# Kernel tuning notes

Hardware: AMD Instinct MI355X
Metric: run time of the kernel (lower is better)

The kernel has to match this reference:

```python
import jax, jax.numpy as jnp
import numpy as np

N_NODES = 10000
N_EDGES = 100000
DIM = 768
NEG_SLOPE = 0.2  # PyG GATConv default


def gat_conv(x, src, dst, W, att_src, att_dst, bias, num_nodes):
    """Single-head PyG-style GATConv. src/dst already include self-loops."""
    h = x @ W                                  # [N, D]
    a_s = h @ att_src                          # [N]
    a_d = h @ att_dst                          # [N]
    e = jax.nn.leaky_relu(a_s[src] + a_d[dst], NEG_SLOPE)  # [E']
    # segment softmax over edges sharing the same destination node
    m = jax.ops.segment_max(e, dst, num_segments=num_nodes)  # [N]
    e = jnp.exp(e - m[dst])
    denom = jax.ops.segment_sum(e, dst, num_segments=num_nodes)  # [N]
    alpha = e / denom[dst]                     # [E']
    msg = alpha[:, None] * h[src]              # [E', D]
    out = jax.ops.segment_sum(msg, dst, num_segments=num_nodes)  # [N, D]
    return out + bias


def setup_inputs() -> dict:
    key = jax.random.key(0)
    ks = jax.random.split(key, 12)
    s = 1.0 / np.sqrt(DIM)
    inp = {
        "x": jax.random.normal(ks[0], (N_NODES, DIM), dtype=jnp.float32),
        "edge_index": jax.random.randint(ks[1], (2, N_EDGES), 0, N_NODES, dtype=jnp.int64),
        "W1": jax.random.normal(ks[2], (DIM, DIM), dtype=jnp.float32) * s,
        "att_src1": jax.random.normal(ks[3], (DIM,), dtype=jnp.float32) * s,
        "att_dst1": jax.random.normal(ks[4], (DIM,), dtype=jnp.float32) * s,
        "b1": jnp.zeros((DIM,), dtype=jnp.float32),
        "W2": jax.random.normal(ks[5], (DIM, DIM), dtype=jnp.float32) * s,
        "att_src2": jax.random.normal(ks[6], (DIM,), dtype=jnp.float32) * s,
        "att_dst2": jax.random.normal(ks[7], (DIM,), dtype=jnp.float32) * s,
        "b2": jnp.zeros((DIM,), dtype=jnp.float32),
    }
    return inp


def reference(x, edge_index, W1, att_src1, att_dst1, b1, W2, att_src2, att_dst2, b2):
    n = x.shape[0]
    # PyG GATConv default add_self_loops=True
    loops = jnp.arange(n, dtype=edge_index.dtype)
    src = jnp.concatenate([edge_index[0], loops])
    dst = jnp.concatenate([edge_index[1], loops])
    h = gat_conv(x, src, dst, W1, att_src1, att_dst1, b1, n)
    h = jax.nn.relu(h)
    # dropout p=0.0 in eval -> identity
    out = gat_conv(h, src, dst, W2, att_src2, att_dst2, b2, n)
    return out
```

## Files before the change

### kernel.cpp

```cpp
#include <hip/hip_runtime.h>

#define DIM 768
#define NEG_SLOPE 0.2f
#define MAXDEG 64

typedef unsigned short ushort_t;
typedef short short8 __attribute__((ext_vector_type(8)));
typedef float floatx4 __attribute__((ext_vector_type(4)));

__device__ __forceinline__ ushort_t f32_to_bf16(float f) {
  unsigned int b = __float_as_uint(f);
  b += 0x7FFFu + ((b >> 16) & 1u);
  return (ushort_t)(b >> 16);
}
__device__ __forceinline__ float bf16_to_f32(ushort_t u) {
  return __uint_as_float(((unsigned int)u) << 16);
}
__device__ __forceinline__ float bf16lo(unsigned int u) {
  return __uint_as_float(u << 16);
}
__device__ __forceinline__ float bf16hi(unsigned int u) {
  return __uint_as_float(u & 0xFFFF0000u);
}
__device__ __forceinline__ unsigned int pack_bf16x2(float lo, float hi) {
  return ((unsigned int)f32_to_bf16(lo)) | (((unsigned int)f32_to_bf16(hi)) << 16);
}

__device__ __forceinline__ void gl2lds16(const ushort_t* g, ushort_t* l) {
  __builtin_amdgcn_global_load_lds(
      (const __attribute__((address_space(1))) void*)g,
      (__attribute__((address_space(3))) void*)l, 16, 0, 0);
}

__global__ __launch_bounds__(256)
void prep_kernel(const float* __restrict__ x, ushort_t* __restrict__ xb, int n4,
                 const float* __restrict__ W1, ushort_t* __restrict__ wT1,
                 const float* __restrict__ W2, ushort_t* __restrict__ wT2,
                 int* __restrict__ zbase, int nz4) {
  __shared__ ushort_t tile[64][65];
  int b = blockIdx.x;
  int t = threadIdx.x;
  if (b < 288) {
    int mat = b / 144;
    int ti = b - mat * 144;
    int tr = (ti / 12) * 64;
    int tc = (ti % 12) * 64;
    const float* W = mat ? W2 : W1;
    ushort_t* wT = mat ? wT2 : wT1;
    int lr = t >> 4, lc4 = (t & 15) * 4;
#pragma unroll
    for (int p = 0; p < 4; ++p) {
      int row = lr + p * 16;
      float4 v = *(const float4*)(W + (size_t)(tr + row) * DIM + tc + lc4);
      tile[row][lc4 + 0] = f32_to_bf16(v.x);
      tile[row][lc4 + 1] = f32_to_bf16(v.y);
      tile[row][lc4 + 2] = f32_to_bf16(v.z);
      tile[row][lc4 + 3] = f32_to_bf16(v.w);
    }
    __syncthreads();
    int n = t & 63, kb = (t >> 6) * 16;
    ushort_t tmp[16];
#pragma unroll
    for (int i = 0; i < 16; ++i) tmp[i] = tile[kb + i][n];
    ushort_t* dst = wT + (size_t)(tc + n) * DIM + tr + kb;
    *(uint4*)(dst) = *(const uint4*)(&tmp[0]);
    *(uint4*)(dst + 8) = *(const uint4*)(&tmp[8]);
  } else {
    int i = (b - 288) * 256 + t;
    if (i < n4) {
      float4 v = ((const float4*)x)[i];
      ushort4 o;
      o.x = f32_to_bf16(v.x); o.y = f32_to_bf16(v.y);
      o.z = f32_to_bf16(v.z); o.w = f32_to_bf16(v.w);
      ((ushort4*)xb)[i] = o;
    }
    if (i < nz4) {
      ((uint4*)zbase)[i] = make_uint4(0, 0, 0, 0);
    }
  }
}

__global__ void csr_kernel(const int* __restrict__ ei, int* __restrict__ deg,
                           int* __restrict__ col, int E, int Etot) {
  int e = blockIdx.x * 256 + threadIdx.x;
  if (e >= Etot) return;
  int s, d;
  if (e < E) { s = ei[e]; d = ei[E + e]; }
  else       { s = e - E; d = e - E; }
  int slot = atomicAdd(&deg[d], 1);
  if (slot < MAXDEG) col[(size_t)d * MAXDEG + slot] = s;
}

__global__ __launch_bounds__(256)
void gemm_kernel(const ushort_t* __restrict__ A, const ushort_t* __restrict__ Bt,
                 const float* __restrict__ att_s, const float* __restrict__ att_d,
                 float* __restrict__ a_s, float* __restrict__ a_d,
                 ushort_t* __restrict__ Hb, int M, int MBLK) {
  const int K = DIM;
  __shared__ __align__(16) ushort_t As[2][128 * 64];
  __shared__ __align__(16) ushort_t Bs[2][128 * 64];
  int b = blockIdx.x;
  int x = b & 7, sidx = b >> 3;
  int m_local = sidx / 6, nblk = sidx - m_local * 6;
  int mblk = x * MBLK + m_local;
  if (mblk * 128 >= M) return;
  int m0 = mblk * 128, n0 = nblk * 128;
  int tid = threadIdx.x;
  int wave = tid >> 6, lane = tid & 63;
  int quad = lane >> 4, l16 = lane & 15;
  int wr = wave >> 1, wc = wave & 1;

  floatx4 acc[4][4];
  const floatx4 fzero = {0.f, 0.f, 0.f, 0.f};
#pragma unroll
  for (int i = 0; i < 4; ++i)
#pragma unroll
    for (int j = 0; j < 4; ++j) acc[i][j] = fzero;

  int lr = lane >> 3, lc = lane & 7;
  const ushort_t* gA[4];
  const ushort_t* gB[4];
  ushort_t* lA[4];
  ushort_t* lB[4];
#pragma unroll
  for (int t = 0; t < 4; ++t) {
    int r = t * 32 + wave * 8 + lr;
    int g = lc ^ (r & 7);
    gA[t] = A + (size_t)min(m0 + r, M - 1) * K + g * 8;
    gB[t] = Bt + (size_t)(n0 + r) * K + g * 8;
    lA[t] = &As[0][(t * 32 + wave * 8) * 64];
    lB[t] = &Bs[0][(t * 32 + wave * 8) * 64];
  }

#define GEMM_STAGE(k0_, buf_)                                         \
  {                                                                   \
    _Pragma("unroll")                                                 \
    for (int t = 0; t < 4; ++t) gl2lds16(gA[t] + (k0_), lA[t] + (buf_)*8192); \
    _Pragma("unroll")                                                 \
    for (int t = 0; t < 4; ++t) gl2lds16(gB[t] + (k0_), lB[t] + (buf_)*8192); \
  }

  GEMM_STAGE(0, 0);
  __syncthreads();
  int cur = 0;

  for (int k0 = 0; k0 < K; k0 += 64) {
    if (k0 + 64 < K) GEMM_STAGE(k0 + 64, cur ^ 1);
    const ushort_t* Ab = &As[cur][0];
    const ushort_t* Bb = &Bs[cur][0];
#pragma unroll
    for (int h = 0; h < 2; ++h) {
      short8 af[4], bfr[4];
#pragma unroll
      for (int i = 0; i < 4; ++i) {
        int ra = wr * 64 + i * 16 + l16;
        af[i] = *(const short8*)(Ab + ra * 64 + ((((h << 2) | quad)) ^ (ra & 7)) * 8);
      }
#pragma unroll
      for (int j = 0; j < 4; ++j) {
        int rb = wc * 64 + j * 16 + l16;
        bfr[j] = *(const short8*)(Bb + rb * 64 + ((((h << 2) | quad)) ^ (rb & 7)) * 8);
      }
#pragma unroll
      for (int i = 0; i < 4; ++i)
#pragma unroll
        for (int j = 0; j < 4; ++j)
          acc[i][j] = __builtin_amdgcn_mfma_f32_16x16x32_bf16(af[i], bfr[j], acc[i][j], 0, 0, 0);
    }
    __syncthreads();
    cur ^= 1;
  }

  float avs[4], avd[4];
#pragma unroll
  for (int j = 0; j < 4; ++j) {
    int c = n0 + wc * 64 + j * 16 + l16;
    avs[j] = att_s[c];
    avd[j] = att_d[c];
  }

#pragma unroll
  for (int i = 0; i < 4; ++i) {
#pragma unroll
    for (int r2 = 0; r2 < 4; ++r2) {
      int row = m0 + wr * 64 + i * 16 + quad * 4 + r2;
      bool valid = row < M;
      float pvs = 0.f, pvd = 0.f;
#pragma unroll
      for (int j = 0; j < 4; ++j) {
        float v = acc[i][j][r2];
        if (valid) Hb[(size_t)row * DIM + n0 + wc * 64 + j * 16 + l16] = f32_to_bf16(v);
        pvs = fmaf(v, avs[j], pvs);
        pvd = fmaf(v, avd[j], pvd);
      }
#pragma unroll
      for (int off = 1; off < 16; off <<= 1) {
        pvs += __shfl_xor(pvs, off, 64);
        pvd += __shfl_xor(pvd, off, 64);
      }
      if (valid && l16 == 0) {
        atomicAdd(a_s + row, pvs);
        atomicAdd(a_d + row, pvd);
      }
    }
  }
}

__global__ __launch_bounds__(256)
void aggregate_kernel(const ushort_t* __restrict__ h, const float* __restrict__ a_s,
                      const float* __restrict__ a_d, const int* __restrict__ deg,
                      const int* __restrict__ col, const float* __restrict__ bias,
                      float* __restrict__ out_f32, ushort_t* __restrict__ out_bf16,
                      int relu_mode, int N) {
  int wave = threadIdx.x >> 6, lane = threadIdx.x & 63;
  int node = blockIdx.x * 4 + wave;
  if (node >= N) return;
  int dg = min(deg[node], MAXDEG);
  int base = node * MAXDEG;
  float ad = a_d[node];

  bool has = lane < dg;
  int sc = col[base + min(lane, dg - 1)];
  float v = a_s[sc] + ad;
  v = (v > 0.f) ? v : NEG_SLOPE * v;
  float vmax = v;
#pragma unroll
  for (int off = 32; off > 0; off >>= 1) vmax = fmaxf(vmax, __shfl_xor(vmax, off, 64));
  float ex = has ? __expf(v - vmax) : 0.f;
  float ssum = ex;
#pragma unroll
  for (int off = 32; off > 0; off >>= 1) ssum += __shfl_xor(ssum, off, 64);
  float al = ex * (1.f / ssum);

  float acc8[8];
  float acc4[4];
#pragma unroll
  for (int k = 0; k < 8; ++k) acc8[k] = 0.f;
#pragma unroll
  for (int k = 0; k < 4; ++k) acc4[k] = 0.f;

  uint4 uA[4], uB[4];
  ushort4 tA[4], tB[4];
  float wA[4], wB[4];

#define GAT_LOADC(b_, u_, t_, w_)                                     \
  {                                                                   \
    _Pragma("unroll")                                                 \
    for (int q = 0; q < 4; ++q) {                                     \
      int j_ = (b_) + q;                                              \
      w_[q] = __shfl(al, j_, 64);                                     \
      int s_ = __shfl(sc, j_, 64);                                    \
      const ushort_t* hr_ = h + (size_t)s_ * DIM;                     \
      u_[q] = *(const uint4*)(hr_ + lane * 8);                        \
      t_[q] = *(const ushort4*)(hr_ + 512 + lane * 4);                \
    }                                                                 \
  }

#define GAT_FMAC(u_, t_, w_)                                          \
  {                                                                   \
    _Pragma("unroll")                                                 \
    for (int q = 0; q < 4; ++q) {                                     \
      float w = w_[q];                                                \
      acc8[0] = fmaf(w, bf16lo(u_[q].x), acc8[0]);                    \
      acc8[1] = fmaf(w, bf16hi(u_[q].x), acc8[1]);                    \
      acc8[2] = fmaf(w, bf16lo(u_[q].y), acc8[2]);                    \
      acc8[3] = fmaf(w, bf16hi(u_[q].y), acc8[3]);                    \
      acc8[4] = fmaf(w, bf16lo(u_[q].z), acc8[4]);                    \
      acc8[5] = fmaf(w, bf16hi(u_[q].z), acc8[5]);                    \
      acc8[6] = fmaf(w, bf16lo(u_[q].w), acc8[6]);                    \
      acc8[7] = fmaf(w, bf16hi(u_[q].w), acc8[7]);                    \
      acc4[0] = fmaf(w, bf16_to_f32(t_[q].x), acc4[0]);               \
      acc4[1] = fmaf(w, bf16_to_f32(t_[q].y), acc4[1]);               \
      acc4[2] = fmaf(w, bf16_to_f32(t_[q].z), acc4[2]);               \
      acc4[3] = fmaf(w, bf16_to_f32(t_[q].w), acc4[3]);               \
    }                                                                 \
  }

  int dgc = (dg + 3) & ~3;
  GAT_LOADC(0, uA, tA, wA);
  for (int b = 0; b < dgc; b += 8) {
    if (b + 4 < dgc) GAT_LOADC(b + 4, uB, tB, wB);
    GAT_FMAC(uA, tA, wA);
    if (b + 8 < dgc) GAT_LOADC(b + 8, uA, tA, wA);
    if (b + 4 < dgc) GAT_FMAC(uB, tB, wB);
  }

  size_t ob = (size_t)node * DIM;
  int c8 = lane * 8, c4 = 512 + lane * 4;
  float4 b0 = *(const float4*)(bias + c8);
  float4 b1 = *(const float4*)(bias + c8 + 4);
  float4 b2 = *(const float4*)(bias + c4);
  float o[12];
  o[0] = acc8[0] + b0.x; o[1] = acc8[1] + b0.y;
  o[2] = acc8[2] + b0.z; o[3] = acc8[3] + b0.w;
  o[4] = acc8[4] + b1.x; o[5] = acc8[5] + b1.y;
  o[6] = acc8[6] + b1.z; o[7] = acc8[7] + b1.w;
  o[8] = acc4[0] + b2.x; o[9] = acc4[1] + b2.y;
  o[10] = acc4[2] + b2.z; o[11] = acc4[3] + b2.w;
  if (relu_mode) {
#pragma unroll
    for (int k = 0; k < 12; ++k) o[k] = fmaxf(o[k], 0.f);
    uint4 s0;
    s0.x = pack_bf16x2(o[0], o[1]);
    s0.y = pack_bf16x2(o[2], o[3]);
    s0.z = pack_bf16x2(o[4], o[5]);
    s0.w = pack_bf16x2(o[6], o[7]);
    *(uint4*)(out_bf16 + ob + c8) = s0;
    uint2 s1;
    s1.x = pack_bf16x2(o[8], o[9]);
    s1.y = pack_bf16x2(o[10], o[11]);
    *(uint2*)(out_bf16 + ob + c4) = s1;
  } else {
    *(float4*)(out_f32 + ob + c8) = make_float4(o[0], o[1], o[2], o[3]);
    *(float4*)(out_f32 + ob + c8 + 4) = make_float4(o[4], o[5], o[6], o[7]);
    *(float4*)(out_f32 + ob + c4) = make_float4(o[8], o[9], o[10], o[11]);
  }
}

extern "C" void kernel_launch(void* const* d_in, const int* in_sizes, int n_in,
                              void* d_out, int out_size, void* d_ws, size_t ws_size,
                              hipStream_t stream) {
  const float* x   = (const float*)d_in[0];
  const int*   ei  = (const int*)d_in[1];
  const float* W1  = (const float*)d_in[2];
  const float* as1 = (const float*)d_in[3];
  const float* ad1 = (const float*)d_in[4];
  const float* b1  = (const float*)d_in[5];
  const float* W2  = (const float*)d_in[6];
  const float* as2 = (const float*)d_in[7];
  const float* ad2 = (const float*)d_in[8];
  const float* b2  = (const float*)d_in[9];

  const int N = in_sizes[0] / DIM;
  const int E = in_sizes[1] / 2;
  const int Etot = E + N;

  char* p = (char*)d_ws;
  auto alloc = [&](size_t bytes) {
    char* q = p;
    p += (bytes + 255) & ~(size_t)255;
    return q;
  };
  ushort_t* Hb     = (ushort_t*)alloc((size_t)N * DIM * 2);
  ushort_t* xb     = (ushort_t*)alloc((size_t)N * DIM * 2);
  ushort_t* wT1    = (ushort_t*)alloc((size_t)DIM * DIM * 2);
  ushort_t* wT2    = (ushort_t*)alloc((size_t)DIM * DIM * 2);
  int*      zbase  = (int*)alloc((size_t)5 * N * 4 + 16);
  int*      deg    = zbase;
  float*    a_s1   = (float*)(zbase + N);
  float*    a_d1   = (float*)(zbase + 2 * N);
  float*    a_s2   = (float*)(zbase + 3 * N);
  float*    a_d2   = (float*)(zbase + 4 * N);
  int*      col    = (int*)alloc((size_t)N * MAXDEG * 4);

  int n4 = N * DIM / 4;
  int nz4 = (5 * N + 3) / 4;
  int prep_blocks = 288 + (n4 + 255) / 256;
  prep_kernel<<<prep_blocks, 256, 0, stream>>>(x, xb, n4, W1, wT1, W2, wT2,
                                               zbase, nz4);
  csr_kernel<<<(Etot + 255) / 256, 256, 0, stream>>>(ei, deg, col, E, Etot);

  int MB = (N + 127) / 128;
  int MBLK = (MB + 7) / 8;
  int gemm_blocks = 8 * MBLK * 6;
  int agg_blocks = (N + 3) / 4;

  gemm_kernel<<<gemm_blocks, 256, 0, stream>>>(xb, wT1, as1, ad1, a_s1, a_d1, Hb, N, MBLK);
  aggregate_kernel<<<agg_blocks, 256, 0, stream>>>(Hb, a_s1, a_d1, deg, col, b1,
                                                   nullptr, xb, 1, N);
  gemm_kernel<<<gemm_blocks, 256, 0, stream>>>(xb, wT2, as2, ad2, a_s2, a_d2, Hb, N, MBLK);
  aggregate_kernel<<<agg_blocks, 256, 0, stream>>>(Hb, a_s2, a_d2, deg, col, b2,
                                                   (float*)d_out, nullptr, 0, N);
}
```

Measured before the change: 200.5 us.

## Fold CSR build into GEMM launch and split aggregation into alpha and gather

CSR construction now runs as extra blocks of the first GEMM launch, which removes one launch and lets the edge scatter overlap the matmul. Aggregation is split into two kernels: one computes the softmax weights per node and stores them, plus padded column indices, in a new alpha buffer. A persistent-style gather kernel with half the blocks then loops over nodes and prefetches the next node's degree, columns and weights while accumulating the current one. This adds one launch per layer and extra global traffic for the alpha array, in exchange for overlapping the softmax and index loads with the gather.

```diff
diff --git a/kernel.cpp b/kernel.cpp
--- a/kernel.cpp
+++ b/kernel.cpp
@@ -80,26 +80,28 @@
   }
 }
 
-__global__ void csr_kernel(const int* __restrict__ ei, int* __restrict__ deg,
-                           int* __restrict__ col, int E, int Etot) {
-  int e = blockIdx.x * 256 + threadIdx.x;
-  if (e >= Etot) return;
-  int s, d;
-  if (e < E) { s = ei[e]; d = ei[E + e]; }
-  else       { s = e - E; d = e - E; }
-  int slot = atomicAdd(&deg[d], 1);
-  if (slot < MAXDEG) col[(size_t)d * MAXDEG + slot] = s;
-}
-
 __global__ __launch_bounds__(256)
 void gemm_kernel(const ushort_t* __restrict__ A, const ushort_t* __restrict__ Bt,
                  const float* __restrict__ att_s, const float* __restrict__ att_d,
                  float* __restrict__ a_s, float* __restrict__ a_d,
-                 ushort_t* __restrict__ Hb, int M, int MBLK) {
+                 ushort_t* __restrict__ Hb, int M, int MBLK,
+                 const int* __restrict__ ei, int* __restrict__ degw,
+                 int* __restrict__ colw, int E, int Etot, int gemmBlocks) {
   const int K = DIM;
   __shared__ __align__(16) ushort_t As[2][128 * 64];
   __shared__ __align__(16) ushort_t Bs[2][128 * 64];
   int b = blockIdx.x;
+  if (b >= gemmBlocks) {
+    int e = (b - gemmBlocks) * 256 + threadIdx.x;
+    if (e < Etot) {
+      int s, d;
+      if (e < E) { s = ei[e]; d = ei[E + e]; }
+      else       { s = e - E; d = e - E; }
+      int slot = atomicAdd(&degw[d], 1);
+      if (slot < MAXDEG) colw[(size_t)d * MAXDEG + slot] = s;
+    }
+    return;
+  }
   int x = b & 7, sidx = b >> 3;
   int m_local = sidx / 6, nblk = sidx - m_local * 6;
   int mblk = x * MBLK + m_local;
@@ -207,11 +209,9 @@
 }
 
 __global__ __launch_bounds__(256)
-void aggregate_kernel(const ushort_t* __restrict__ h, const float* __restrict__ a_s,
-                      const float* __restrict__ a_d, const int* __restrict__ deg,
-                      const int* __restrict__ col, const float* __restrict__ bias,
-                      float* __restrict__ out_f32, ushort_t* __restrict__ out_bf16,
-                      int relu_mode, int N) {
+void alpha_kernel(const float* __restrict__ a_s, const float* __restrict__ a_d,
+                  const int* __restrict__ deg, int* __restrict__ col,
+                  float* __restrict__ alpha, int N) {
   int wave = threadIdx.x >> 6, lane = threadIdx.x & 63;
   int node = blockIdx.x * 4 + wave;
   if (node >= N) return;
@@ -230,14 +230,24 @@
   float ssum = ex;
 #pragma unroll
   for (int off = 32; off > 0; off >>= 1) ssum += __shfl_xor(ssum, off, 64);
-  float al = ex * (1.f / ssum);
-
-  float acc8[8];
-  float acc4[4];
-#pragma unroll
-  for (int k = 0; k < 8; ++k) acc8[k] = 0.f;
-#pragma unroll
-  for (int k = 0; k < 4; ++k) acc4[k] = 0.f;
+  alpha[base + lane] = ex * (1.f / ssum);
+  if (!has) col[base + lane] = sc;
+}
+
+__global__ __launch_bounds__(256)
+void gather_kernel(const ushort_t* __restrict__ h, const float* __restrict__ alpha,
+                   const int* __restrict__ deg, const int* __restrict__ col,
+                   const float* __restrict__ bias,
+                   float* __restrict__ out_f32, ushort_t* __restrict__ out_bf16,
+                   int relu_mode, int N) {
+  int lane = threadIdx.x & 63;
+  int wstride = gridDim.x * 4;
+  int node = blockIdx.x * 4 + (threadIdx.x >> 6);
+  if (node >= N) return;
+
+  int dg = min(deg[node], MAXDEG);
+  int sc = col[node * MAXDEG + lane];
+  float al = alpha[node * MAXDEG + lane];
 
   uint4 uA[4], uB[4];
   ushort4 tA[4], tB[4];
@@ -276,44 +286,66 @@
     }                                                                 \
   }
 
-  int dgc = (dg + 3) & ~3;
-  GAT_LOADC(0, uA, tA, wA);
-  for (int b = 0; b < dgc; b += 8) {
-    if (b + 4 < dgc) GAT_LOADC(b + 4, uB, tB, wB);
-    GAT_FMAC(uA, tA, wA);
-    if (b + 8 < dgc) GAT_LOADC(b + 8, uA, tA, wA);
-    if (b + 4 < dgc) GAT_FMAC(uB, tB, wB);
-  }
-
-  size_t ob = (size_t)node * DIM;
   int c8 = lane * 8, c4 = 512 + lane * 4;
   float4 b0 = *(const float4*)(bias + c8);
   float4 b1 = *(const float4*)(bias + c8 + 4);
   float4 b2 = *(const float4*)(bias + c4);
-  float o[12];
-  o[0] = acc8[0] + b0.x; o[1] = acc8[1] + b0.y;
-  o[2] = acc8[2] + b0.z; o[3] = acc8[3] + b0.w;
-  o[4] = acc8[4] + b1.x; o[5] = acc8[5] + b1.y;
-  o[6] = acc8[6] + b1.z; o[7] = acc8[7] + b1.w;
-  o[8] = acc4[0] + b2.x; o[9] = acc4[1] + b2.y;
-  o[10] = acc4[2] + b2.z; o[11] = acc4[3] + b2.w;
-  if (relu_mode) {
-#pragma unroll
-    for (int k = 0; k < 12; ++k) o[k] = fmaxf(o[k], 0.f);
-    uint4 s0;
-    s0.x = pack_bf16x2(o[0], o[1]);
-    s0.y = pack_bf16x2(o[2], o[3]);
-    s0.z = pack_bf16x2(o[4], o[5]);
-    s0.w = pack_bf16x2(o[6], o[7]);
-    *(uint4*)(out_bf16 + ob + c8) = s0;
-    uint2 s1;
-    s1.x = pack_bf16x2(o[8], o[9]);
-    s1.y = pack_bf16x2(o[10], o[11]);
-    *(uint2*)(out_bf16 + ob + c4) = s1;
-  } else {
-    *(float4*)(out_f32 + ob + c8) = make_float4(o[0], o[1], o[2], o[3]);
-    *(float4*)(out_f32 + ob + c8 + 4) = make_float4(o[4], o[5], o[6], o[7]);
-    *(float4*)(out_f32 + ob + c4) = make_float4(o[8], o[9], o[10], o[11]);
+
+  while (node < N) {
+    int nn = node + wstride;
+    float acc8[8];
+    float acc4[4];
+#pragma unroll
+    for (int k = 0; k < 8; ++k) acc8[k] = 0.f;
+#pragma unroll
+    for (int k = 0; k < 4; ++k) acc4[k] = 0.f;
+
+    int dgc = (dg + 3) & ~3;
+    GAT_LOADC(0, uA, tA, wA);
+
+    int dg2 = 0, sc2 = 0;
+    float al2 = 0.f;
+    if (nn < N) {
+      dg2 = min(deg[nn], MAXDEG);
+      sc2 = col[nn * MAXDEG + lane];
+      al2 = alpha[nn * MAXDEG + lane];
+    }
+
+    for (int b = 0; b < dgc; b += 8) {
+      if (b + 4 < dgc) GAT_LOADC(b + 4, uB, tB, wB);
+      GAT_FMAC(uA, tA, wA);
+      if (b + 8 < dgc) GAT_LOADC(b + 8, uA, tA, wA);
+      if (b + 4 < dgc) GAT_FMAC(uB, tB, wB);
+    }
+
+    size_t ob = (size_t)node * DIM;
+    float o[12];
+    o[0] = acc8[0] + b0.x; o[1] = acc8[1] + b0.y;
+    o[2] = acc8[2] + b0.z; o[3] = acc8[3] + b0.w;
+    o[4] = acc8[4] + b1.x; o[5] = acc8[5] + b1.y;
+    o[6] = acc8[6] + b1.z; o[7] = acc8[7] + b1.w;
+    o[8] = acc4[0] + b2.x; o[9] = acc4[1] + b2.y;
+    o[10] = acc4[2] + b2.z; o[11] = acc4[3] + b2.w;
+    if (relu_mode) {
+#pragma unroll
+      for (int k = 0; k < 12; ++k) o[k] = fmaxf(o[k], 0.f);
+      uint4 s0;
+      s0.x = pack_bf16x2(o[0], o[1]);
+      s0.y = pack_bf16x2(o[2], o[3]);
+      s0.z = pack_bf16x2(o[4], o[5]);
+      s0.w = pack_bf16x2(o[6], o[7]);
+      *(uint4*)(out_bf16 + ob + c8) = s0;
+      uint2 s1;
+      s1.x = pack_bf16x2(o[8], o[9]);
+      s1.y = pack_bf16x2(o[10], o[11]);
+      *(uint2*)(out_bf16 + ob + c4) = s1;
+    } else {
+      *(float4*)(out_f32 + ob + c8) = make_float4(o[0], o[1], o[2], o[3]);
+      *(float4*)(out_f32 + ob + c8 + 4) = make_float4(o[4], o[5], o[6], o[7]);
+      *(float4*)(out_f32 + ob + c4) = make_float4(o[8], o[9], o[10], o[11]);
+    }
+
+    node = nn; dg = dg2; sc = sc2; al = al2;
   }
 }
 
@@ -352,23 +384,29 @@
   float*    a_s2   = (float*)(zbase + 3 * N);
   float*    a_d2   = (float*)(zbase + 4 * N);
   int*      col    = (int*)alloc((size_t)N * MAXDEG * 4);
+  float*    alpha  = (float*)alloc((size_t)N * MAXDEG * 4);
 
   int n4 = N * DIM / 4;
   int nz4 = (5 * N + 3) / 4;
   int prep_blocks = 288 + (n4 + 255) / 256;
   prep_kernel<<<prep_blocks, 256, 0, stream>>>(x, xb, n4, W1, wT1, W2, wT2,
                                                zbase, nz4);
-  csr_kernel<<<(Etot + 255) / 256, 256, 0, stream>>>(ei, deg, col, E, Etot);
 
   int MB = (N + 127) / 128;
   int MBLK = (MB + 7) / 8;
   int gemm_blocks = 8 * MBLK * 6;
-  int agg_blocks = (N + 3) / 4;
-
-  gemm_kernel<<<gemm_blocks, 256, 0, stream>>>(xb, wT1, as1, ad1, a_s1, a_d1, Hb, N, MBLK);
-  aggregate_kernel<<<agg_blocks, 256, 0, stream>>>(Hb, a_s1, a_d1, deg, col, b1,
+  int csr_blocks = (Etot + 255) / 256;
+  int alpha_blocks = (N + 3) / 4;
+  int gather_blocks = (N + 7) / 8;
+
+  gemm_kernel<<<gemm_blocks + csr_blocks, 256, 0, stream>>>(
+      xb, wT1, as1, ad1, a_s1, a_d1, Hb, N, MBLK, ei, deg, col, E, Etot, gemm_blocks);
+  alpha_kernel<<<alpha_blocks, 256, 0, stream>>>(a_s1, a_d1, deg, col, alpha, N);
+  gather_kernel<<<gather_blocks, 256, 0, stream>>>(Hb, alpha, deg, col, b1,
                                                    nullptr, xb, 1, N);
-  gemm_kernel<<<gemm_blocks, 256, 0, stream>>>(xb, wT2, as2, ad2, a_s2, a_d2, Hb, N, MBLK);
-  aggregate_kernel<<<agg_blocks, 256, 0, stream>>>(Hb, a_s2, a_d2, deg, col, b2,
+  gemm_kernel<<<gemm_blocks, 256, 0, stream>>>(
+      xb, wT2, as2, ad2, a_s2, a_d2, Hb, N, MBLK, ei, deg, col, E, 0, gemm_blocks);
+  alpha_kernel<<<alpha_blocks, 256, 0, stream>>>(a_s2, a_d2, deg, col, alpha, N);
+  gather_kernel<<<gather_blocks, 256, 0, stream>>>(Hb, alpha, deg, col, b2,
                                                    (float*)d_out, nullptr, 0, N);
 }
```

Result: slower. 207.2 us (+3.3%).

## Fuse all GAT stages into one persistent kernel with grid barriers

Applied to the files above, without the earlier changes.

Replaces the six separate kernel launches (prep, CSR build, two GEMMs, two aggregations) with a single persistent mega-kernel that steps through the phases using a software grid-wide barrier. Zeroing of the degree and attention buffers moves to a hipMemsetAsync. The aim is to remove launch gaps and inter-kernel drain/fill costs. In exchange, the GEMM and aggregation phases become grid-stride loops over a fixed grid, which changes occupancy and load balance. The spin barrier is also only safe if all blocks are co-resident, and the grid size (G = 8*MBLK*6, 480 blocks here) is not checked against residency limits.

```diff
diff --git a/kernel.cpp b/kernel.cpp
--- a/kernel.cpp
+++ b/kernel.cpp
@@ -32,105 +32,78 @@
       (__attribute__((address_space(3))) void*)l, 16, 0, 0);
 }
 
-__global__ __launch_bounds__(256)
-void prep_kernel(const float* __restrict__ x, ushort_t* __restrict__ xb, int n4,
-                 const float* __restrict__ W1, ushort_t* __restrict__ wT1,
-                 const float* __restrict__ W2, ushort_t* __restrict__ wT2,
-                 int* __restrict__ zbase, int nz4) {
-  __shared__ ushort_t tile[64][65];
-  int b = blockIdx.x;
-  int t = threadIdx.x;
-  if (b < 288) {
-    int mat = b / 144;
-    int ti = b - mat * 144;
-    int tr = (ti / 12) * 64;
-    int tc = (ti % 12) * 64;
-    const float* W = mat ? W2 : W1;
-    ushort_t* wT = mat ? wT2 : wT1;
-    int lr = t >> 4, lc4 = (t & 15) * 4;
-#pragma unroll
-    for (int p = 0; p < 4; ++p) {
-      int row = lr + p * 16;
-      float4 v = *(const float4*)(W + (size_t)(tr + row) * DIM + tc + lc4);
-      tile[row][lc4 + 0] = f32_to_bf16(v.x);
-      tile[row][lc4 + 1] = f32_to_bf16(v.y);
-      tile[row][lc4 + 2] = f32_to_bf16(v.z);
-      tile[row][lc4 + 3] = f32_to_bf16(v.w);
-    }
-    __syncthreads();
-    int n = t & 63, kb = (t >> 6) * 16;
-    ushort_t tmp[16];
-#pragma unroll
-    for (int i = 0; i < 16; ++i) tmp[i] = tile[kb + i][n];
-    ushort_t* dst = wT + (size_t)(tc + n) * DIM + tr + kb;
-    *(uint4*)(dst) = *(const uint4*)(&tmp[0]);
-    *(uint4*)(dst + 8) = *(const uint4*)(&tmp[8]);
-  } else {
-    int i = (b - 288) * 256 + t;
-    if (i < n4) {
-      float4 v = ((const float4*)x)[i];
-      ushort4 o;
-      o.x = f32_to_bf16(v.x); o.y = f32_to_bf16(v.y);
-      o.z = f32_to_bf16(v.z); o.w = f32_to_bf16(v.w);
-      ((ushort4*)xb)[i] = o;
-    }
-    if (i < nz4) {
-      ((uint4*)zbase)[i] = make_uint4(0, 0, 0, 0);
-    }
-  }
-}
-
-__global__ void csr_kernel(const int* __restrict__ ei, int* __restrict__ deg,
-                           int* __restrict__ col, int E, int Etot) {
-  int e = blockIdx.x * 256 + threadIdx.x;
-  if (e >= Etot) return;
-  int s, d;
-  if (e < E) { s = ei[e]; d = ei[E + e]; }
-  else       { s = e - E; d = e - E; }
-  int slot = atomicAdd(&deg[d], 1);
-  if (slot < MAXDEG) col[(size_t)d * MAXDEG + slot] = s;
-}
-
-__global__ __launch_bounds__(256)
-void gemm_kernel(const ushort_t* __restrict__ A, const ushort_t* __restrict__ Bt,
-                 const float* __restrict__ att_s, const float* __restrict__ att_d,
-                 float* __restrict__ a_s, float* __restrict__ a_d,
-                 ushort_t* __restrict__ Hb, int M, int MBLK) {
+__device__ __forceinline__ void grid_barrier(int* cnt, int* gen, int nblk) {
+  __syncthreads();
+  if (threadIdx.x == 0) {
+    __threadfence();
+    int g = __hip_atomic_load(gen, __ATOMIC_ACQUIRE, __HIP_MEMORY_SCOPE_AGENT);
+    int arrived = __hip_atomic_fetch_add(cnt, 1, __ATOMIC_ACQ_REL,
+                                         __HIP_MEMORY_SCOPE_AGENT);
+    if (arrived == nblk - 1) {
+      __hip_atomic_store(cnt, 0, __ATOMIC_RELAXED, __HIP_MEMORY_SCOPE_AGENT);
+      __hip_atomic_store(gen, g + 1, __ATOMIC_RELEASE, __HIP_MEMORY_SCOPE_AGENT);
+    } else {
+      while (__hip_atomic_load(gen, __ATOMIC_ACQUIRE,
+                               __HIP_MEMORY_SCOPE_AGENT) == g) {
+        __builtin_amdgcn_s_sleep(8);
+      }
+    }
+    __threadfence();
+  }
+  __syncthreads();
+}
+
+struct MegaArgs {
+  const float* x; const int* ei;
+  const float* W1; const float* as1; const float* ad1; const float* b1;
+  const float* W2; const float* as2; const float* ad2; const float* b2;
+  ushort_t* xb; ushort_t* wT1; ushort_t* wT2; ushort_t* Hb;
+  int* zbase; int* col;
+  float* out;
+  int N, E, Etot, MBLK, n4;
+};
+
+__device__ __forceinline__ void gemm_phase(
+    const ushort_t* __restrict__ A, const ushort_t* __restrict__ Bt,
+    const float* __restrict__ att_s, const float* __restrict__ att_d,
+    float* __restrict__ a_s, float* __restrict__ a_d,
+    ushort_t* __restrict__ Hb, int M, int MBLK,
+    ushort_t* AsBase, ushort_t* BsBase) {
   const int K = DIM;
-  __shared__ __align__(16) ushort_t As[2][128 * 64];
-  __shared__ __align__(16) ushort_t Bs[2][128 * 64];
-  int b = blockIdx.x;
-  int x = b & 7, sidx = b >> 3;
-  int m_local = sidx / 6, nblk = sidx - m_local * 6;
-  int mblk = x * MBLK + m_local;
-  if (mblk * 128 >= M) return;
-  int m0 = mblk * 128, n0 = nblk * 128;
+  int ntiles = 8 * MBLK * 6;
   int tid = threadIdx.x;
   int wave = tid >> 6, lane = tid & 63;
   int quad = lane >> 4, l16 = lane & 15;
   int wr = wave >> 1, wc = wave & 1;
-
-  floatx4 acc[4][4];
-  const floatx4 fzero = {0.f, 0.f, 0.f, 0.f};
-#pragma unroll
-  for (int i = 0; i < 4; ++i)
-#pragma unroll
-    for (int j = 0; j < 4; ++j) acc[i][j] = fzero;
-
   int lr = lane >> 3, lc = lane & 7;
-  const ushort_t* gA[4];
-  const ushort_t* gB[4];
-  ushort_t* lA[4];
-  ushort_t* lB[4];
-#pragma unroll
-  for (int t = 0; t < 4; ++t) {
-    int r = t * 32 + wave * 8 + lr;
-    int g = lc ^ (r & 7);
-    gA[t] = A + (size_t)min(m0 + r, M - 1) * K + g * 8;
-    gB[t] = Bt + (size_t)(n0 + r) * K + g * 8;
-    lA[t] = &As[0][(t * 32 + wave * 8) * 64];
-    lB[t] = &Bs[0][(t * 32 + wave * 8) * 64];
-  }
+
+  for (int b = blockIdx.x; b < ntiles; b += gridDim.x) {
+    int x = b & 7, sidx = b >> 3;
+    int m_local = sidx / 6, nblk = sidx - m_local * 6;
+    int mblk = x * MBLK + m_local;
+    if (mblk * 128 >= M) continue;
+    int m0 = mblk * 128, n0 = nblk * 128;
+
+    floatx4 acc[4][4];
+    const floatx4 fzero = {0.f, 0.f, 0.f, 0.f};
+#pragma unroll
+    for (int i = 0; i < 4; ++i)
+#pragma unroll
+      for (int j = 0; j < 4; ++j) acc[i][j] = fzero;
+
+    const ushort_t* gA[4];
+    const ushort_t* gB[4];
+    ushort_t* lA[4];
+    ushort_t* lB[4];
+#pragma unroll
+    for (int t = 0; t < 4; ++t) {
+      int r = t * 32 + wave * 8 + lr;
+      int g = lc ^ (r & 7);
+      gA[t] = A + (size_t)min(m0 + r, M - 1) * K + g * 8;
+      gB[t] = Bt + (size_t)(n0 + r) * K + g * 8;
+      lA[t] = AsBase + (t * 32 + wave * 8) * 64;
+      lB[t] = BsBase + (t * 32 + wave * 8) * 64;
+    }
 
 #define GEMM_STAGE(k0_, buf_)                                         \
   {                                                                   \
@@ -140,108 +113,117 @@
     for (int t = 0; t < 4; ++t) gl2lds16(gB[t] + (k0_), lB[t] + (buf_)*8192); \
   }
 
-  GEMM_STAGE(0, 0);
-  __syncthreads();
-  int cur = 0;
-
-  for (int k0 = 0; k0 < K; k0 += 64) {
-    if (k0 + 64 < K) GEMM_STAGE(k0 + 64, cur ^ 1);
-    const ushort_t* Ab = &As[cur][0];
-    const ushort_t* Bb = &Bs[cur][0];
-#pragma unroll
-    for (int h = 0; h < 2; ++h) {
-      short8 af[4], bfr[4];
-#pragma unroll
-      for (int i = 0; i < 4; ++i) {
-        int ra = wr * 64 + i * 16 + l16;
-        af[i] = *(const short8*)(Ab + ra * 64 + ((((h << 2) | quad)) ^ (ra & 7)) * 8);
+    GEMM_STAGE(0, 0);
+    __syncthreads();
+    int cur = 0;
+
+    for (int k0 = 0; k0 < K; k0 += 64) {
+      if (k0 + 64 < K) GEMM_STAGE(k0 + 64, cur ^ 1);
+      const ushort_t* Ab = AsBase + cur * 8192;
+      const ushort_t* Bb = BsBase + cur * 8192;
+#pragma unroll
+      for (int h = 0; h < 2; ++h) {
+        short8 af[4], bfr[4];
+#pragma unroll
+        for (int i = 0; i < 4; ++i) {
+          int ra = wr * 64 + i * 16 + l16;
+          af[i] = *(const short8*)(Ab + ra * 64 + ((((h << 2) | quad)) ^ (ra & 7)) * 8);
+        }
+#pragma unroll
+        for (int j = 0; j < 4; ++j) {
+          int rb = wc * 64 + j * 16 + l16;
+          bfr[j] = *(const short8*)(Bb + rb * 64 + ((((h << 2) | quad)) ^ (rb & 7)) * 8);
+        }
+#pragma unroll
+        for (int i = 0; i < 4; ++i)
+#pragma unroll
+          for (int j = 0; j < 4; ++j)
+            acc[i][j] = __builtin_amdgcn_mfma_f32_16x16x32_bf16(af[i], bfr[j], acc[i][j], 0, 0, 0);
       }
-#pragma unroll
-      for (int j = 0; j < 4; ++j) {
-        int rb = wc * 64 + j * 16 + l16;
-        bfr[j] = *(const short8*)(Bb + rb * 64 + ((((h << 2) | quad)) ^ (rb & 7)) * 8);
+      __syncthreads();
+      cur ^= 1;
+    }
+#undef GEMM_STAGE
+
+    float avs[4], avd[4];
+#pragma unroll
+    for (int j = 0; j < 4; ++j) {
+      int c = n0 + wc * 64 + j * 16 + l16;
+      avs[j] = att_s[c];
+      avd[j] = att_d[c];
+    }
+
+#pragma unroll
+    for (int i = 0; i < 4; ++i) {
+#pragma unroll
+      for (int r2 = 0; r2 < 4; ++r2) {
+        int row = m0 + wr * 64 + i * 16 + quad * 4 + r2;
+        bool valid = row < M;
+        float pvs = 0.f, pvd = 0.f;
+#pragma unroll
+        for (int j = 0; j < 4; ++j) {
+          float v = acc[i][j][r2];
+          if (valid) Hb[(size_t)row * DIM + n0 + wc * 64 + j * 16 + l16] = f32_to_bf16(v);
+          pvs = fmaf(v, avs[j], pvs);
+          pvd = fmaf(v, avd[j], pvd);
+        }
+#pragma unroll
+        for (int off = 1; off < 16; off <<= 1) {
+          pvs += __shfl_xor(pvs, off, 64);
+          pvd += __shfl_xor(pvd, off, 64);
+        }
+        if (valid && l16 == 0) {
+          atomicAdd(a_s + row, pvs);
+          atomicAdd(a_d + row, pvd);
+        }
       }
-#pragma unroll
-      for (int i = 0; i < 4; ++i)
-#pragma unroll
-        for (int j = 0; j < 4; ++j)
-          acc[i][j] = __builtin_amdgcn_mfma_f32_16x16x32_bf16(af[i], bfr[j], acc[i][j], 0, 0, 0);
-    }
-    __syncthreads();
-    cur ^= 1;
-  }
-
-  float avs[4], avd[4];
-#pragma unroll
-  for (int j = 0; j < 4; ++j) {
-    int c = n0 + wc * 64 + j * 16 + l16;
-    avs[j] = att_s[c];
-    avd[j] = att_d[c];
-  }
-
-#pragma unroll
-  for (int i = 0; i < 4; ++i) {
-#pragma unroll
-    for (int r2 = 0; r2 < 4; ++r2) {
-      int row = m0 + wr * 64 + i * 16 + quad * 4 + r2;
-      bool valid = row < M;
-      float pvs = 0.f, pvd = 0.f;
-#pragma unroll
-      for (int j = 0; j < 4; ++j) {
-        float v = acc[i][j][r2];
-        if (valid) Hb[(size_t)row * DIM + n0 + wc * 64 + j * 16 + l16] = f32_to_bf16(v);
-        pvs = fmaf(v, avs[j], pvs);
-        pvd = fmaf(v, avd[j], pvd);
-      }
-#pragma unroll
-      for (int off = 1; off < 16; off <<= 1) {
-        pvs += __shfl_xor(pvs, off, 64);
-        pvd += __shfl_xor(pvd, off, 64);
-      }
-      if (valid && l16 == 0) {
-        atomicAdd(a_s + row, pvs);
-        atomicAdd(a_d + row, pvd);
-      }
-    }
-  }
-}
-
-__global__ __launch_bounds__(256)
-void aggregate_kernel(const ushort_t* __restrict__ h, const float* __restrict__ a_s,
-                      const float* __restrict__ a_d, const int* __restrict__ deg,
-                      const int* __restrict__ col, const float* __restrict__ bias,
-                      float* __restrict__ out_f32, ushort_t* __restrict__ out_bf16,
-                      int relu_mode, int N) {
-  int wave = threadIdx.x >> 6, lane = threadIdx.x & 63;
-  int node = blockIdx.x * 4 + wave;
-  if (node >= N) return;
-  int dg = min(deg[node], MAXDEG);
-  int base = node * MAXDEG;
-  float ad = a_d[node];
-
-  bool has = lane < dg;
-  int sc = col[base + min(lane, dg - 1)];
-  float v = a_s[sc] + ad;
-  v = (v > 0.f) ? v : NEG_SLOPE * v;
-  float vmax = v;
-#pragma unroll
-  for (int off = 32; off > 0; off >>= 1) vmax = fmaxf(vmax, __shfl_xor(vmax, off, 64));
-  float ex = has ? __expf(v - vmax) : 0.f;
-  float ssum = ex;
-#pragma unroll
-  for (int off = 32; off > 0; off >>= 1) ssum += __shfl_xor(ssum, off, 64);
-  float al = ex * (1.f / ssum);
-
-  float acc8[8];
-  float acc4[4];
-#pragma unroll
-  for (int k = 0; k < 8; ++k) acc8[k] = 0.f;
-#pragma unroll
-  for (int k = 0; k < 4; ++k) acc4[k] = 0.f;
-
-  uint4 uA[4], uB[4];
-  ushort4 tA[4], tB[4];
-  float wA[4], wB[4];
+    }
+  }
+}
+
+__device__ __forceinline__ void agg_phase(
+    const ushort_t* __restrict__ h, const float* __restrict__ a_s,
+    float* a_d, int* deg,
+    const int* __restrict__ col, const float* __restrict__ bias,
+    float* __restrict__ out_f32, ushort_t* __restrict__ out_bf16,
+    int relu_mode, int N) {
+  int lane = threadIdx.x & 63;
+  int wave = threadIdx.x >> 6;
+  int c8 = lane * 8, c4 = 512 + lane * 4;
+  float4 b0 = *(const float4*)(bias + c8);
+  float4 b1v = *(const float4*)(bias + c8 + 4);
+  float4 b2v = *(const float4*)(bias + c4);
+
+  for (int node = blockIdx.x * 4 + wave; node < N; node += gridDim.x * 4) {
+    int dg = min(__hip_atomic_load(&deg[node], __ATOMIC_RELAXED,
+                                   __HIP_MEMORY_SCOPE_AGENT), MAXDEG);
+    int base = node * MAXDEG;
+    float ad = __hip_atomic_load(&a_d[node], __ATOMIC_RELAXED,
+                                 __HIP_MEMORY_SCOPE_AGENT);
+
+    bool has = lane < dg;
+    int sc = col[base + min(lane, dg - 1)];
+    float v = a_s[sc] + ad;
+    v = (v > 0.f) ? v : NEG_SLOPE * v;
+    float vmax = v;
+#pragma unroll
+    for (int off = 32; off > 0; off >>= 1) vmax = fmaxf(vmax, __shfl_xor(vmax, off, 64));
+    float ex = has ? __expf(v - vmax) : 0.f;
+    float ssum = ex;
+#pragma unroll
+    for (int off = 32; off > 0; off >>= 1) ssum += __shfl_xor(ssum, off, 64);
+    float al = ex * (1.f / ssum);
+
+    float acc8[8];
+    float acc4[4];
+#pragma unroll
+    for (int k = 0; k < 8; ++k) acc8[k] = 0.f;
+#pragma unroll
+    for (int k = 0; k < 4; ++k) acc4[k] = 0.f;
+
+    uint4 uA[4], uB[4];
+    ushort4 tA[4], tB[4];
+    float wA[4], wB[4];
 
 #define GAT_LOADC(b_, u_, t_, w_)                                     \
   {                                                                   \
@@ -276,45 +258,121 @@
     }                                                                 \
   }
 
-  int dgc = (dg + 3) & ~3;
-  GAT_LOADC(0, uA, tA, wA);
-  for (int b = 0; b < dgc; b += 8) {
-    if (b + 4 < dgc) GAT_LOADC(b + 4, uB, tB, wB);
-    GAT_FMAC(uA, tA, wA);
-    if (b + 8 < dgc) GAT_LOADC(b + 8, uA, tA, wA);
-    if (b + 4 < dgc) GAT_FMAC(uB, tB, wB);
-  }
-
-  size_t ob = (size_t)node * DIM;
-  int c8 = lane * 8, c4 = 512 + lane * 4;
-  float4 b0 = *(const float4*)(bias + c8);
-  float4 b1 = *(const float4*)(bias + c8 + 4);
-  float4 b2 = *(const float4*)(bias + c4);
-  float o[12];
-  o[0] = acc8[0] + b0.x; o[1] = acc8[1] + b0.y;
-  o[2] = acc8[2] + b0.z; o[3] = acc8[3] + b0.w;
-  o[4] = acc8[4] + b1.x; o[5] = acc8[5] + b1.y;
-  o[6] = acc8[6] + b1.z; o[7] = acc8[7] + b1.w;
-  o[8] = acc4[0] + b2.x; o[9] = acc4[1] + b2.y;
-  o[10] = acc4[2] + b2.z; o[11] = acc4[3] + b2.w;
-  if (relu_mode) {
-#pragma unroll
-    for (int k = 0; k < 12; ++k) o[k] = fmaxf(o[k], 0.f);
-    uint4 s0;
-    s0.x = pack_bf16x2(o[0], o[1]);
-    s0.y = pack_bf16x2(o[2], o[3]);
-    s0.z = pack_bf16x2(o[4], o[5]);
-    s0.w = pack_bf16x2(o[6], o[7]);
-    *(uint4*)(out_bf16 + ob + c8) = s0;
-    uint2 s1;
-    s1.x = pack_bf16x2(o[8], o[9]);
-    s1.y = pack_bf16x2(o[10], o[11]);
-    *(uint2*)(out_bf16 + ob + c4) = s1;
-  } else {
-    *(float4*)(out_f32 + ob + c8) = make_float4(o[0], o[1], o[2], o[3]);
-    *(float4*)(out_f32 + ob + c8 + 4) = make_float4(o[4], o[5], o[6], o[7]);
-    *(float4*)(out_f32 + ob + c4) = make_float4(o[8], o[9], o[10], o[11]);
-  }
+    int dgc = (dg + 3) & ~3;
+    GAT_LOADC(0, uA, tA, wA);
+    for (int bb = 0; bb < dgc; bb += 8) {
+      if (bb + 4 < dgc) GAT_LOADC(bb + 4, uB, tB, wB);
+      GAT_FMAC(uA, tA, wA);
+      if (bb + 8 < dgc) GAT_LOADC(bb + 8, uA, tA, wA);
+      if (bb + 4 < dgc) GAT_FMAC(uB, tB, wB);
+    }
+#undef GAT_LOADC
+#undef GAT_FMAC
+
+    size_t ob = (size_t)node * DIM;
+    float o[12];
+    o[0] = acc8[0] + b0.x; o[1] = acc8[1] + b0.y;
+    o[2] = acc8[2] + b0.z; o[3] = acc8[3] + b0.w;
+    o[4] = acc8[4] + b1v.x; o[5] = acc8[5] + b1v.y;
+    o[6] = acc8[6] + b1v.z; o[7] = acc8[7] + b1v.w;
+    o[8] = acc4[0] + b2v.x; o[9] = acc4[1] + b2v.y;
+    o[10] = acc4[2] + b2v.z; o[11] = acc4[3] + b2v.w;
+    if (relu_mode) {
+#pragma unroll
+      for (int k = 0; k < 12; ++k) o[k] = fmaxf(o[k], 0.f);
+      uint4 s0;
+      s0.x = pack_bf16x2(o[0], o[1]);
+      s0.y = pack_bf16x2(o[2], o[3]);
+      s0.z = pack_bf16x2(o[4], o[5]);
+      s0.w = pack_bf16x2(o[6], o[7]);
+      *(uint4*)(out_bf16 + ob + c8) = s0;
+      uint2 s1;
+      s1.x = pack_bf16x2(o[8], o[9]);
+      s1.y = pack_bf16x2(o[10], o[11]);
+      *(uint2*)(out_bf16 + ob + c4) = s1;
+    } else {
+      *(float4*)(out_f32 + ob + c8) = make_float4(o[0], o[1], o[2], o[3]);
+      *(float4*)(out_f32 + ob + c8 + 4) = make_float4(o[4], o[5], o[6], o[7]);
+      *(float4*)(out_f32 + ob + c4) = make_float4(o[8], o[9], o[10], o[11]);
+    }
+  }
+}
+
+__global__ __launch_bounds__(256, 2)
+void mega_kernel(MegaArgs a) {
+  __shared__ __align__(16) ushort_t As[2][128 * 64];
+  __shared__ __align__(16) ushort_t Bs[2][128 * 64];
+
+  int* deg    = a.zbase;
+  float* a_s1 = (float*)(a.zbase + a.N);
+  float* a_d1 = (float*)(a.zbase + 2 * a.N);
+  float* a_s2 = (float*)(a.zbase + 3 * a.N);
+  float* a_d2 = (float*)(a.zbase + 4 * a.N);
+  int* bcnt   = a.zbase + 5 * a.N;
+  int* bgen   = a.zbase + 5 * a.N + 1;
+  int nblk    = gridDim.x;
+
+  {
+    ushort_t (*tile)[65] = reinterpret_cast<ushort_t(*)[65]>(&As[0][0]);
+    int t = threadIdx.x;
+    for (int b = blockIdx.x; b < 288; b += gridDim.x) {
+      int mat = b / 144;
+      int ti = b - mat * 144;
+      int tr = (ti / 12) * 64;
+      int tc = (ti % 12) * 64;
+      const float* W = mat ? a.W2 : a.W1;
+      ushort_t* wT = mat ? a.wT2 : a.wT1;
+      int lr = t >> 4, lc4 = (t & 15) * 4;
+#pragma unroll
+      for (int p = 0; p < 4; ++p) {
+        int row = lr + p * 16;
+        float4 v = *(const float4*)(W + (size_t)(tr + row) * DIM + tc + lc4);
+        tile[row][lc4 + 0] = f32_to_bf16(v.x);
+        tile[row][lc4 + 1] = f32_to_bf16(v.y);
+        tile[row][lc4 + 2] = f32_to_bf16(v.z);
+        tile[row][lc4 + 3] = f32_to_bf16(v.w);
+      }
+      __syncthreads();
+      int n = t & 63, kb = (t >> 6) * 16;
+      ushort_t tmp[16];
+#pragma unroll
+      for (int i = 0; i < 16; ++i) tmp[i] = tile[kb + i][n];
+      ushort_t* dst = wT + (size_t)(tc + n) * DIM + tr + kb;
+      *(uint4*)(dst) = *(const uint4*)(&tmp[0]);
+      *(uint4*)(dst + 8) = *(const uint4*)(&tmp[8]);
+      __syncthreads();
+    }
+    for (int i = blockIdx.x * 256 + threadIdx.x; i < a.n4; i += gridDim.x * 256) {
+      float4 v = ((const float4*)a.x)[i];
+      ushort4 o;
+      o.x = f32_to_bf16(v.x); o.y = f32_to_bf16(v.y);
+      o.z = f32_to_bf16(v.z); o.w = f32_to_bf16(v.w);
+      ((ushort4*)a.xb)[i] = o;
+    }
+  }
+  grid_barrier(bcnt, bgen, nblk);
+
+  for (int e = blockIdx.x * 256 + threadIdx.x; e < a.Etot; e += gridDim.x * 256) {
+    int s, d;
+    if (e < a.E) { s = a.ei[e]; d = a.ei[a.E + e]; }
+    else         { s = e - a.E; d = e - a.E; }
+    int slot = atomicAdd(&deg[d], 1);
+    if (slot < MAXDEG) a.col[(size_t)d * MAXDEG + slot] = s;
+  }
+  grid_barrier(bcnt, bgen, nblk);
+
+  gemm_phase(a.xb, a.wT1, a.as1, a.ad1, a_s1, a_d1, a.Hb, a.N, a.MBLK,
+             &As[0][0], &Bs[0][0]);
+  grid_barrier(bcnt, bgen, nblk);
+
+  agg_phase(a.Hb, a_s1, a_d1, deg, a.col, a.b1, nullptr, a.xb, 1, a.N);
+  grid_barrier(bcnt, bgen, nblk);
+
+  gemm_phase(a.xb, a.wT2, a.as2, a.ad2, a_s2, a_d2, a.Hb, a.N, a.MBLK,
+             &As[0][0], &Bs[0][0]);
+  grid_barrier(bcnt, bgen, nblk);
+
+  agg_phase(a.Hb, a_s2, a_d2, deg, a.col, a.b2, a.out, nullptr, 0, a.N);
 }
 
 extern "C" void kernel_launch(void* const* d_in, const int* in_sizes, int n_in,
@@ -346,29 +404,22 @@
   ushort_t* wT1    = (ushort_t*)alloc((size_t)DIM * DIM * 2);
   ushort_t* wT2    = (ushort_t*)alloc((size_t)DIM * DIM * 2);
   int*      zbase  = (int*)alloc((size_t)5 * N * 4 + 16);
-  int*      deg    = zbase;
-  float*    a_s1   = (float*)(zbase + N);
-  float*    a_d1   = (float*)(zbase + 2 * N);
-  float*    a_s2   = (float*)(zbase + 3 * N);
-  float*    a_d2   = (float*)(zbase + 4 * N);
   int*      col    = (int*)alloc((size_t)N * MAXDEG * 4);
-
-  int n4 = N * DIM / 4;
-  int nz4 = (5 * N + 3) / 4;
-  int prep_blocks = 288 + (n4 + 255) / 256;
-  prep_kernel<<<prep_blocks, 256, 0, stream>>>(x, xb, n4, W1, wT1, W2, wT2,
-                                               zbase, nz4);
-  csr_kernel<<<(Etot + 255) / 256, 256, 0, stream>>>(ei, deg, col, E, Etot);
 
   int MB = (N + 127) / 128;
   int MBLK = (MB + 7) / 8;
-  int gemm_blocks = 8 * MBLK * 6;
-  int agg_blocks = (N + 3) / 4;
-
-  gemm_kernel<<<gemm_blocks, 256, 0, stream>>>(xb, wT1, as1, ad1, a_s1, a_d1, Hb, N, MBLK);
-  aggregate_kernel<<<agg_blocks, 256, 0, stream>>>(Hb, a_s1, a_d1, deg, col, b1,
-                                                   nullptr, xb, 1, N);
-  gemm_kernel<<<gemm_blocks, 256, 0, stream>>>(xb, wT2, as2, ad2, a_s2, a_d2, Hb, N, MBLK);
-  aggregate_kernel<<<agg_blocks, 256, 0, stream>>>(Hb, a_s2, a_d2, deg, col, b2,
-                                                   (float*)d_out, nullptr, 0, N);
-}
+  int G = 8 * MBLK * 6;
+
+  MegaArgs a;
+  a.x = x; a.ei = ei;
+  a.W1 = W1; a.as1 = as1; a.ad1 = ad1; a.b1 = b1;
+  a.W2 = W2; a.as2 = as2; a.ad2 = ad2; a.b2 = b2;
+  a.xb = xb; a.wT1 = wT1; a.wT2 = wT2; a.Hb = Hb;
+  a.zbase = zbase; a.col = col;
+  a.out = (float*)d_out;
+  a.N = N; a.E = E; a.Etot = Etot; a.MBLK = MBLK;
+  a.n4 = N * DIM / 4;
+
+  hipMemsetAsync(zbase, 0, (size_t)5 * N * 4 + 16, stream);
+  mega_kernel<<<G, 256, 0, stream>>>(a);
+}
```

New measurement: 686.2 us. 242% more time.
